# Kernel optimization log

Hardware: AMD Instinct MI355X
Metric: run time of the kernel (lower is better)

Reference implementation:

```python
import jax, jax.numpy as jnp
import numpy as np

N_HEAD = 16
EPS = 1e-6

def hypersphere_norm(x, g):
    # unit-normalize on hidden dim, rescale to sqrt(d), learnable gain
    d = x.shape[-1]
    n = jnp.linalg.norm(x, axis=-1, keepdims=True)
    return (x / (n + EPS)) * jnp.sqrt(jnp.asarray(d, x.dtype)) * g


def setup_inputs() -> dict:
    key = jax.random.key(0)
    ks = jax.random.split(key, 8)
    B, S, D, F = 2, 2048, 2048, 8192
    s = lambda fan: 1.0 / np.sqrt(fan)
    return {
        "hidden_states": jax.random.normal(ks[0], (B, S, D), jnp.float32),
        "Wq": jax.random.normal(ks[1], (D, D), jnp.float32) * s(D),
        "Wk": jax.random.normal(ks[2], (D, D), jnp.float32) * s(D),
        "Wv": jax.random.normal(ks[3], (D, D), jnp.float32) * s(D),
        "Wo": jax.random.normal(ks[4], (D, D), jnp.float32) * s(D),
        "W_in": jax.random.normal(ks[5], (F, D), jnp.float32) * s(D),
        "W_out": jax.random.normal(ks[6], (D, F), jnp.float32) * s(F),
        "qk_norm_factor": jnp.asarray(1.0 / np.sqrt(D // N_HEAD), jnp.float32),
        "g_attn": jnp.ones((D,), jnp.float32),
        "g_mlp": jnp.ones((D,), jnp.float32),
    }


def reference(hidden_states, Wq, Wk, Wv, Wo, W_in, W_out, qk_norm_factor, g_attn, g_mlp):
    B, S, D = hidden_states.shape
    H = N_HEAD
    hd = D // H

    # ---- pre-attn hypersphere norm ----
    residual = hidden_states
    x = hypersphere_norm(hidden_states, g_attn)

    def shape_heads(t):  # [B,S,D] -> [B,H,S,hd]
        return t.reshape(B, S, H, hd).transpose(0, 2, 1, 3)

    q = shape_heads(x @ Wq.T)
    k = shape_heads(x @ Wk.T)
    v = shape_heads(x @ Wv.T)

    # QK-norm: unit-normalize per head vector
    q = q / (jnp.linalg.norm(q, axis=-1, keepdims=True) + EPS)
    k = k / (jnp.linalg.norm(k, axis=-1, keepdims=True) + EPS)

    scores = jnp.einsum("bhqd,bhkd->bhqk", q, k) * qk_norm_factor
    causal = jnp.tril(jnp.ones((S, S), bool))
    scores = jnp.where(causal[None, None], scores, jnp.asarray(-jnp.inf, scores.dtype))
    probs = jax.nn.softmax(scores, axis=-1)
    attn = jnp.einsum("bhqk,bhkd->bhqd", probs, v)  # [B,H,S,hd]
    attn = attn.transpose(0, 2, 1, 3).reshape(B, S, D)
    attn = attn @ Wo.T  # dropout=0

    h = residual + attn

    # ---- MLP branch ----
    residual = h
    y = hypersphere_norm(h, g_mlp)
    y = jax.nn.gelu(y @ W_in.T, approximate=False)
    y = y @ W_out.T
    return residual + y
```

## Files before the change

### kernel.cpp

```cpp
#include <hip/hip_runtime.h>
#include <math.h>


typedef unsigned short ushort_t;
typedef __attribute__((ext_vector_type(8))) short short8;
typedef __attribute__((ext_vector_type(4))) short short4v;
typedef __attribute__((ext_vector_type(4))) float f32x4;

#define S_LEN 2048
#define D_DIM 2048
#define F_DIM 8192
#define NHEAD 16
#define HDIM 128
#define BATCH 2
#define MROWS (BATCH * S_LEN)

__device__ __forceinline__ float bf2f(ushort_t u) {
  union { unsigned int i; float f; } c; c.i = ((unsigned int)u) << 16; return c.f;
}
__device__ __forceinline__ ushort_t f2bf(float f) {
  union { unsigned int i; float f; } c; c.f = f;
  unsigned int u = c.i;
  unsigned int r = (u + 0x7FFFu + ((u >> 16) & 1u)) >> 16;
  return (ushort_t)r;
}
__device__ __forceinline__ void load_lds16(const ushort_t* g, ushort_t* l) {
  __builtin_amdgcn_global_load_lds((const __attribute__((address_space(1))) void*)g,
                                   (__attribute__((address_space(3))) void*)l,
                                   16, 0, 0);
}
__device__ __forceinline__ f32x4 mf(short8 a, short8 b, f32x4 c) {
  return __builtin_amdgcn_mfma_f32_16x16x32_bf16(a, b, c, 0, 0, 0);
}

__global__ __launch_bounds__(256) void f2b_all_kernel(const float* __restrict__ wq,
                                                      const float* __restrict__ wk,
                                                      const float* __restrict__ wv,
                                                      const float* __restrict__ wo,
                                                      const float* __restrict__ wi,
                                                      const float* __restrict__ wu,
                                                      ushort_t* __restrict__ out) {
  const size_t DD = (size_t)D_DIM * D_DIM;
  const size_t FD = (size_t)F_DIM * D_DIM;
  const size_t e = ((size_t)blockIdx.x * 256 + threadIdx.x) * 4;
  const float* src;
  size_t off;
  if (e < 4 * DD) {
    const int wsel = (int)(e >> 22);
    src = (wsel == 0) ? wq : (wsel == 1) ? wk : (wsel == 2) ? wv : wo;
    off = e & (DD - 1);
  } else if (e < 4 * DD + FD) {
    src = wi; off = e - 4 * DD;
  } else {
    src = wu; off = e - 4 * DD - FD;
  }
  float4 v = *(const float4*)(src + off);
  short4v o;
  o[0] = (short)f2bf(v.x); o[1] = (short)f2bf(v.y);
  o[2] = (short)f2bf(v.z); o[3] = (short)f2bf(v.w);
  *(short4v*)(out + e) = o;
}

__global__ __launch_bounds__(256) void hsnorm_kernel(const float* __restrict__ x,
                                                     const float* __restrict__ g,
                                                     ushort_t* __restrict__ out) {
  const int row = blockIdx.x;
  const int t = threadIdx.x;
  const size_t base = (size_t)row * D_DIM + t * 8;
  float4 x0 = *(const float4*)(x + base);
  float4 x1 = *(const float4*)(x + base + 4);
  float f[8] = {x0.x, x0.y, x0.z, x0.w, x1.x, x1.y, x1.z, x1.w};
  float ss = 0.f;
#pragma unroll
  for (int j = 0; j < 8; ++j) ss += f[j] * f[j];
#pragma unroll
  for (int o = 32; o >= 1; o >>= 1) ss += __shfl_xor(ss, o);
  __shared__ float red[4];
  if ((t & 63) == 0) red[t >> 6] = ss;
  __syncthreads();
  const float tot = red[0] + red[1] + red[2] + red[3];
  const float factor = 45.254833995939045f / (sqrtf(tot) + 1e-6f);
  float4 g0 = *(const float4*)(g + t * 8);
  float4 g1 = *(const float4*)(g + t * 8 + 4);
  float gg[8] = {g0.x, g0.y, g0.z, g0.w, g1.x, g1.y, g1.z, g1.w};
  short8 ov;
#pragma unroll
  for (int j = 0; j < 8; ++j) ov[j] = (short)f2bf(f[j] * factor * gg[j]);
  *(short8*)(out + base) = ov;
}

__global__ __launch_bounds__(256) void qknorm_kernel(ushort_t* __restrict__ buf, float scale) {
  const int wv = threadIdx.x >> 6;
  const int lane = threadIdx.x & 63;
  const size_t vi = (size_t)blockIdx.x * 4 + wv;
  ushort_t* p = buf + vi * 128 + lane * 2;
  const float a = bf2f(p[0]), b = bf2f(p[1]);
  float ss = a * a + b * b;
#pragma unroll
  for (int o = 32; o >= 1; o >>= 1) ss += __shfl_xor(ss, o);
  const float f = scale / (sqrtf(ss) + 1e-6f);
  p[0] = f2bf(a * f);
  p[1] = f2bf(b * f);
}

template <int EPI>
__global__ __launch_bounds__(512, 2) void gemm256(const ushort_t* __restrict__ A,
                                                  const ushort_t* __restrict__ W,
                                                  const float* __restrict__ RES,
                                                  void* __restrict__ Cv,
                                                  int M, int N, int K) {
  extern __shared__ char smem[];
  const int tid = threadIdx.x;
  const int w = tid >> 6;
  const int lane = tid & 63;
  const int quad = lane >> 4;
  const int l15 = lane & 15;
  const int wr = w >> 2, wc = w & 3;
  const long bm = (long)blockIdx.x * 256;
  const long bn = (long)blockIdx.y * 256;

  const int sw = l15 & 7;
  const int arow = (wr * 128 + l15) << 7;
  const int a_off0 = arow + ((quad ^ sw) << 4);
  const int a_off1 = arow + (((4 | quad) ^ sw) << 4);
  const int brow = (wc * 64 + l15) << 7;
  const int b_off0 = 65536 + brow + ((quad ^ sw) << 4);
  const int b_off1 = 65536 + brow + (((4 | quad) ^ sw) << 4);

  const int sr = tid >> 3;
  const int ss = ((tid & 7) ^ (sr & 7)) << 3;
  const ushort_t* gA = A + (size_t)(bm + sr) * K + ss;
  const ushort_t* gB = W + (size_t)(bn + sr) * K + ss;
  const size_t rstep = (size_t)64 * K;
  const int sdst = w * 1024;

#define STAGE_A(PB, GP)                                                        \
  {                                                                            \
    _Pragma("unroll") for (int ld = 0; ld < 4; ++ld)                           \
        load_lds16((GP) + ld * rstep,                                          \
                   (ushort_t*)(smem + (PB)*32768 + ld * 8192 + sdst));         \
  }
#define STAGE_B(PB, GP)                                                        \
  {                                                                            \
    _Pragma("unroll") for (int ld = 0; ld < 4; ++ld)                           \
        load_lds16((GP) + ld * rstep,                                          \
                   (ushort_t*)(smem + 65536 + (PB)*32768 + ld * 8192 + sdst)); \
  }

  f32x4 acc[8][4] = {};
  short8 af[4][2], bf[4][2];
  const int NT = K >> 6;

  STAGE_A(0, gA);
  STAGE_B(0, gB);
  STAGE_A(1, gA + 64);
  gA += 128;
  gB += 64;
  asm volatile("s_waitcnt vmcnt(4)" ::: "memory");
  __builtin_amdgcn_s_barrier();

  for (int kt0 = 0; kt0 < NT; kt0 += 2) {
#pragma unroll
    for (int pp = 0; pp < 2; ++pp) {
      const int kt = kt0 + pp;
      const char* sa = smem + pp * 32768;
#pragma unroll
      for (int i = 0; i < 4; ++i) {
        af[i][0] = *(const short8*)(sa + a_off0 + i * 2048);
        af[i][1] = *(const short8*)(sa + a_off1 + i * 2048);
      }
#pragma unroll
      for (int j = 0; j < 2; ++j) {
        bf[j][0] = *(const short8*)(sa + b_off0 + j * 2048);
        bf[j][1] = *(const short8*)(sa + b_off1 + j * 2048);
      }
      if (kt + 1 < NT) STAGE_B(1 - pp, gB);
      gB += 64;
      __builtin_amdgcn_s_barrier();
      __builtin_amdgcn_s_setprio(1);
#pragma unroll
      for (int i = 0; i < 4; ++i)
#pragma unroll
        for (int j = 0; j < 2; ++j) {
          acc[i][j] = mf(af[i][0], bf[j][0], acc[i][j]);
          acc[i][j] = mf(af[i][1], bf[j][1], acc[i][j]);
        }
      __builtin_amdgcn_s_setprio(0);
      __builtin_amdgcn_s_barrier();
#pragma unroll
      for (int j = 0; j < 2; ++j) {
        bf[2 + j][0] = *(const short8*)(sa + b_off0 + (2 + j) * 2048);
        bf[2 + j][1] = *(const short8*)(sa + b_off1 + (2 + j) * 2048);
      }
      __builtin_amdgcn_s_barrier();
      __builtin_amdgcn_s_setprio(1);
#pragma unroll
      for (int i = 0; i < 4; ++i)
#pragma unroll
        for (int j = 0; j < 2; ++j) {
          acc[i][2 + j] = mf(af[i][0], bf[2 + j][0], acc[i][2 + j]);
          acc[i][2 + j] = mf(af[i][1], bf[2 + j][1], acc[i][2 + j]);
        }
      __builtin_amdgcn_s_setprio(0);
      __builtin_amdgcn_s_barrier();
#pragma unroll
      for (int i = 0; i < 4; ++i) {
        af[i][0] = *(const short8*)(sa + a_off0 + (4 + i) * 2048);
        af[i][1] = *(const short8*)(sa + a_off1 + (4 + i) * 2048);
      }
      __builtin_amdgcn_s_barrier();
      __builtin_amdgcn_s_setprio(1);
#pragma unroll
      for (int i = 0; i < 4; ++i)
#pragma unroll
        for (int j = 0; j < 2; ++j) {
          acc[4 + i][2 + j] = mf(af[i][0], bf[2 + j][0], acc[4 + i][2 + j]);
          acc[4 + i][2 + j] = mf(af[i][1], bf[2 + j][1], acc[4 + i][2 + j]);
        }
      __builtin_amdgcn_s_setprio(0);
      __builtin_amdgcn_s_barrier();
      if (kt + 2 < NT) STAGE_A(pp, gA);
      gA += 64;
      __builtin_amdgcn_s_barrier();
      __builtin_amdgcn_s_setprio(1);
#pragma unroll
      for (int i = 0; i < 4; ++i)
#pragma unroll
        for (int j = 0; j < 2; ++j) {
          acc[4 + i][j] = mf(af[i][0], bf[j][0], acc[4 + i][j]);
          acc[4 + i][j] = mf(af[i][1], bf[j][1], acc[4 + i][j]);
        }
      __builtin_amdgcn_s_setprio(0);
      if (kt + 2 < NT) {
        asm volatile("s_waitcnt vmcnt(4)" ::: "memory");
      } else {
        asm volatile("s_waitcnt vmcnt(0)" ::: "memory");
      }
      __builtin_amdgcn_s_barrier();
    }
  }
#undef STAGE_A
#undef STAGE_B

  const size_t SZq = (size_t)MROWS * D_DIM;
#pragma unroll
  for (int i = 0; i < 8; ++i) {
    const long row0 = bm + wr * 128 + i * 16 + quad * 4;
#pragma unroll
    for (int j = 0; j < 4; ++j) {
      const long col = bn + wc * 64 + j * 16 + l15;
      if (EPI == 4) {
        if (col < 4096) {
          ushort_t* dst = (ushort_t*)Cv + (col < 2048 ? 0 : SZq);
          const long c = col & (D_DIM - 1);
#pragma unroll
          for (int r = 0; r < 4; ++r)
            dst[(size_t)(row0 + r) * D_DIM + c] = f2bf(acc[i][j][r]);
        } else {
          const long b = row0 >> 11;
          const long s0 = row0 & (S_LEN - 1);
          const long h = (col >> 7) & 15;
          const long d = col & (HDIM - 1);
          short4v ov;
#pragma unroll
          for (int r = 0; r < 4; ++r) ov[r] = (short)f2bf(acc[i][j][r]);
          *(short4v*)((ushort_t*)Cv + 2 * SZq + ((b * NHEAD + h) * HDIM + d) * S_LEN + s0) = ov;
        }
      } else {
#pragma unroll
        for (int r = 0; r < 4; ++r) {
          float v = acc[i][j][r];
          const size_t idx = (size_t)(row0 + r) * N + col;
          if (EPI == 1) {
            ((float*)Cv)[idx] = v + RES[idx];
          } else if (EPI == 2) {
            v = 0.5f * v * (1.0f + erff(v * 0.70710678118654752f));
            ((ushort_t*)Cv)[idx] = f2bf(v);
          }
        }
      }
    }
  }
}

__global__ __launch_bounds__(256) void attn_kernel(const ushort_t* __restrict__ q,
                                                   const ushort_t* __restrict__ k,
                                                   const ushort_t* __restrict__ vt,
                                                   ushort_t* __restrict__ out) {
  __shared__ __align__(16) ushort_t K_lds[64 * 128];
  __shared__ __align__(16) ushort_t Vt_lds[128 * 64];
  __shared__ __align__(16) ushort_t P_lds[4 * 16 * 64];
  const int tid = threadIdx.x;
  const int w = tid >> 6;
  const int lane = tid & 63;
  const int quad = lane >> 4;
  const int l15 = lane & 15;

  const int qt = (S_LEN / 64 - 1) - (blockIdx.x & (S_LEN / 64 - 1));
  const int bh = blockIdx.x >> 5;
  const int b = bh >> 4;
  const int h = bh & 15;
  const int q0 = qt * 64;
  const int wrow0 = q0 + w * 16;
  const size_t base = ((size_t)b * S_LEN) * D_DIM + h * HDIM;
  const size_t vtbase = ((size_t)(b * NHEAD + h)) * HDIM * S_LEN;

  short8 qa[4];
#pragma unroll
  for (int st = 0; st < 4; ++st)
    qa[st] = *(const short8*)(q + base + (size_t)(wrow0 + l15) * D_DIM + st * 32 + quad * 8);

  const int kc0 = w * 64 + lane;
  ushort_t* Pw = P_lds + w * 1024;

  f32x4 o[8] = {};
  float m[4], l[4];
#pragma unroll
  for (int r = 0; r < 4; ++r) { m[r] = -__builtin_inff(); l[r] = 0.f; }

  const int ktmax = (q0 + 63) >> 6;
  for (int kt = 0; kt <= ktmax; ++kt) {
#pragma unroll
    for (int r2 = 0; r2 < 4; ++r2) {
      const int c = r2 * 256 + kc0;
      {
        const int db = c >> 8, key = (c >> 2) & 63, dl = (c & 3) * 8;
        load_lds16(k + base + (size_t)(kt * 64 + key) * D_DIM + db * 32 + dl,
                   K_lds + (size_t)(r2 * 4 + w) * 512);
      }
      {
        const int kc = c >> 9, d = (c >> 2) & 127, kl = (c & 3) * 8;
        load_lds16(vt + vtbase + (size_t)d * S_LEN + kt * 64 + kc * 32 + kl,
                   Vt_lds + (size_t)(r2 * 4 + w) * 512);
      }
    }
    __syncthreads();

    if (kt * 64 <= wrow0 + 15) {
      f32x4 s[4];
#pragma unroll
      for (int h2 = 0; h2 < 4; ++h2) {
        f32x4 sa = {};
#pragma unroll
        for (int st = 0; st < 4; ++st) {
          short8 kb = *(const short8*)&K_lds[st * 2048 + (h2 * 16 + l15) * 32 + quad * 8];
          sa = __builtin_amdgcn_mfma_f32_16x16x32_bf16(qa[st], kb, sa, 0, 0, 0);
        }
        s[h2] = sa;
      }

      const int kbase = kt * 64 + l15;
      float alpha[4];
#pragma unroll
      for (int r = 0; r < 4; ++r) {
        const int qrow = wrow0 + quad * 4 + r;
        float sv[4];
#pragma unroll
        for (int h2 = 0; h2 < 4; ++h2)
          sv[h2] = (kbase + h2 * 16 <= qrow) ? s[h2][r] : -__builtin_inff();
        float tmax = fmaxf(fmaxf(sv[0], sv[1]), fmaxf(sv[2], sv[3]));
#pragma unroll
        for (int off = 8; off >= 1; off >>= 1) tmax = fmaxf(tmax, __shfl_xor(tmax, off));
        const float mn = fmaxf(m[r], tmax);
        const float al = __expf(m[r] - mn);
        float p[4], ps = 0.f;
#pragma unroll
        for (int h2 = 0; h2 < 4; ++h2) { p[h2] = __expf(sv[h2] - mn); ps += p[h2]; }
#pragma unroll
        for (int off = 8; off >= 1; off >>= 1) ps += __shfl_xor(ps, off);
        l[r] = l[r] * al + ps;
        m[r] = mn;
        alpha[r] = al;
#pragma unroll
        for (int h2 = 0; h2 < 4; ++h2)
          Pw[(h2 >> 1) * 512 + (quad * 4 + r) * 32 + (h2 & 1) * 16 + l15] = f2bf(p[h2]);
      }

#pragma unroll
      for (int c = 0; c < 8; ++c)
#pragma unroll
        for (int r = 0; r < 4; ++r) o[c][r] *= alpha[r];

      short8 af0 = *(const short8*)&Pw[l15 * 32 + quad * 8];
      short8 af1 = *(const short8*)&Pw[512 + l15 * 32 + quad * 8];
#pragma unroll
      for (int c = 0; c < 8; ++c) {
        short8 vb0 = *(const short8*)&Vt_lds[(c * 16 + l15) * 32 + quad * 8];
        o[c] = __builtin_amdgcn_mfma_f32_16x16x32_bf16(af0, vb0, o[c], 0, 0, 0);
        short8 vb1 = *(const short8*)&Vt_lds[4096 + (c * 16 + l15) * 32 + quad * 8];
        o[c] = __builtin_amdgcn_mfma_f32_16x16x32_bf16(af1, vb1, o[c], 0, 0, 0);
      }
    }
    __syncthreads();
  }

#pragma unroll
  for (int c = 0; c < 8; ++c)
#pragma unroll
    for (int r = 0; r < 4; ++r) {
      const float val = o[c][r] / l[r];
      out[base + (size_t)(wrow0 + quad * 4 + r) * D_DIM + c * 16 + l15] = f2bf(val);
    }
}

extern "C" void kernel_launch(void* const* d_in, const int* in_sizes, int n_in,
                              void* d_out, int out_size, void* d_ws, size_t ws_size,
                              hipStream_t stream) {
  const float* hid  = (const float*)d_in[0];
  const float* Wq   = (const float*)d_in[1];
  const float* Wk   = (const float*)d_in[2];
  const float* Wv   = (const float*)d_in[3];
  const float* Wo   = (const float*)d_in[4];
  const float* Win  = (const float*)d_in[5];
  const float* Wout = (const float*)d_in[6];
  const float* ga   = (const float*)d_in[8];
  const float* gm   = (const float*)d_in[9];
  float* out = (float*)d_out;

  const size_t DD = (size_t)D_DIM * D_DIM;
  const size_t FD = (size_t)F_DIM * D_DIM;
  const size_t SZ = (size_t)MROWS * D_DIM;

  ushort_t* wqb  = (ushort_t*)d_ws;
  ushort_t* wob  = wqb + 3 * DD;
  ushort_t* winb = wob + DD;
  ushort_t* woutb= winb + FD;
  float*    hb   = (float*)(woutb + FD);
  ushort_t* qb   = (ushort_t*)(hb + SZ);
  ushort_t* kb   = qb + SZ;
  ushort_t* vtb  = kb + SZ;
  ushort_t* xb   = vtb + SZ;
  ushort_t* mid  = kb;

  static int attr_set = 0;
  if (!attr_set) {
    hipFuncSetAttribute((const void*)&gemm256<1>,
                        hipFuncAttributeMaxDynamicSharedMemorySize, 131072);
    hipFuncSetAttribute((const void*)&gemm256<2>,
                        hipFuncAttributeMaxDynamicSharedMemorySize, 131072);
    hipFuncSetAttribute((const void*)&gemm256<4>,
                        hipFuncAttributeMaxDynamicSharedMemorySize, 131072);
    attr_set = 1;
  }

  f2b_all_kernel<<<(unsigned)((4 * DD + 2 * FD) / 1024), 256, 0, stream>>>(
      Wq, Wk, Wv, Wo, Win, Wout, wqb);

  hsnorm_kernel<<<MROWS, 256, 0, stream>>>(hid, ga, xb);
  gemm256<4><<<dim3(MROWS / 256, 6144 / 256), 512, 131072, stream>>>(
      xb, wqb, nullptr, qb, MROWS, 6144, D_DIM);
  qknorm_kernel<<<(MROWS * NHEAD) / 4, 256, 0, stream>>>(qb, 0.08838834764831845f);
  qknorm_kernel<<<(MROWS * NHEAD) / 4, 256, 0, stream>>>(kb, 1.0f);
  attn_kernel<<<BATCH * NHEAD * (S_LEN / 64), 256, 0, stream>>>(qb, kb, vtb, xb);
  gemm256<1><<<dim3(MROWS / 256, D_DIM / 256), 512, 131072, stream>>>(
      xb, wob, hid, hb, MROWS, D_DIM, D_DIM);
  hsnorm_kernel<<<MROWS, 256, 0, stream>>>(hb, gm, qb);
  gemm256<2><<<dim3(MROWS / 256, F_DIM / 256), 512, 131072, stream>>>(
      qb, winb, nullptr, mid, MROWS, F_DIM, D_DIM);
  gemm256<1><<<dim3(MROWS / 256, D_DIM / 256), 512, 131072, stream>>>(
      mid, woutb, hb, out, MROWS, D_DIM, F_DIM);
}
```

Before: 986.5 us.

## Stage GEMM tiles through registers instead of direct global-to-LDS loads

Replaces the direct global-to-LDS (buffer load to LDS) staging in the GEMM main loop with register-staged loads. A and B tiles are loaded into registers and written to the alternate LDS buffer partway through each k-step. B fragments are now reloaded from LDS instead of kept live, which cuts register pressure. The change reduces LDS buffering depth for A from two tiles ahead to one. It also adds VGPR pressure and exposes global latency within one k-step, and it relies on vmcnt waits the compiler inserts.

```diff
diff --git a/kernel.cpp b/kernel.cpp
--- a/kernel.cpp
+++ b/kernel.cpp
@@ -128,35 +128,28 @@
   const int b_off1 = 65536 + brow + (((4 | quad) ^ sw) << 4);
 
   const int sr = tid >> 3;
-  const int ss = ((tid & 7) ^ (sr & 7)) << 3;
-  const ushort_t* gA = A + (size_t)(bm + sr) * K + ss;
-  const ushort_t* gB = W + (size_t)(bn + sr) * K + ss;
+  const int cs = tid & 7;
+  const ushort_t* gA = A + (size_t)(bm + sr) * K + cs * 8;
+  const ushort_t* gB = W + (size_t)(bn + sr) * K + cs * 8;
   const size_t rstep = (size_t)64 * K;
-  const int sdst = w * 1024;
-
-#define STAGE_A(PB, GP)                                                        \
-  {                                                                            \
-    _Pragma("unroll") for (int ld = 0; ld < 4; ++ld)                           \
-        load_lds16((GP) + ld * rstep,                                          \
-                   (ushort_t*)(smem + (PB)*32768 + ld * 8192 + sdst));         \
-  }
-#define STAGE_B(PB, GP)                                                        \
-  {                                                                            \
-    _Pragma("unroll") for (int ld = 0; ld < 4; ++ld)                           \
-        load_lds16((GP) + ld * rstep,                                          \
-                   (ushort_t*)(smem + 65536 + (PB)*32768 + ld * 8192 + sdst)); \
-  }
+  const int wb = sr * 128 + ((cs ^ (sr & 7)) << 4);
 
   f32x4 acc[8][4] = {};
-  short8 af[4][2], bf[4][2];
+  short8 af[4][2], bf[2][2], aA[4], bB[4];
   const int NT = K >> 6;
 
-  STAGE_A(0, gA);
-  STAGE_B(0, gB);
-  STAGE_A(1, gA + 64);
-  gA += 128;
-  gB += 64;
-  asm volatile("s_waitcnt vmcnt(4)" ::: "memory");
+#pragma unroll
+  for (int ld = 0; ld < 4; ++ld) aA[ld] = *(const short8*)(gA + ld * rstep);
+#pragma unroll
+  for (int ld = 0; ld < 4; ++ld) bB[ld] = *(const short8*)(gB + ld * rstep);
+  gA += 64; gB += 64;
+#pragma unroll
+  for (int ld = 0; ld < 4; ++ld)
+    *(short8*)(smem + wb + ld * 8192) = aA[ld];
+#pragma unroll
+  for (int ld = 0; ld < 4; ++ld)
+    *(short8*)(smem + 65536 + wb + ld * 8192) = bB[ld];
+  asm volatile("s_waitcnt lgkmcnt(0)" ::: "memory");
   __builtin_amdgcn_s_barrier();
 
   for (int kt0 = 0; kt0 < NT; kt0 += 2) {
@@ -164,6 +157,8 @@
     for (int pp = 0; pp < 2; ++pp) {
       const int kt = kt0 + pp;
       const char* sa = smem + pp * 32768;
+      char* wbuf = smem + (1 - pp) * 32768;
+      const bool more = (kt + 1 < NT);
 #pragma unroll
       for (int i = 0; i < 4; ++i) {
         af[i][0] = *(const short8*)(sa + a_off0 + i * 2048);
@@ -174,8 +169,11 @@
         bf[j][0] = *(const short8*)(sa + b_off0 + j * 2048);
         bf[j][1] = *(const short8*)(sa + b_off1 + j * 2048);
       }
-      if (kt + 1 < NT) STAGE_B(1 - pp, gB);
-      gB += 64;
+      if (more) {
+#pragma unroll
+        for (int ld = 0; ld < 4; ++ld) aA[ld] = *(const short8*)(gA + ld * rstep);
+      }
+      gA += 64;
       __builtin_amdgcn_s_barrier();
       __builtin_amdgcn_s_setprio(1);
 #pragma unroll
@@ -189,8 +187,8 @@
       __builtin_amdgcn_s_barrier();
 #pragma unroll
       for (int j = 0; j < 2; ++j) {
-        bf[2 + j][0] = *(const short8*)(sa + b_off0 + (2 + j) * 2048);
-        bf[2 + j][1] = *(const short8*)(sa + b_off1 + (2 + j) * 2048);
+        bf[j][0] = *(const short8*)(sa + b_off0 + (2 + j) * 2048);
+        bf[j][1] = *(const short8*)(sa + b_off1 + (2 + j) * 2048);
       }
       __builtin_amdgcn_s_barrier();
       __builtin_amdgcn_s_setprio(1);
@@ -198,8 +196,8 @@
       for (int i = 0; i < 4; ++i)
 #pragma unroll
         for (int j = 0; j < 2; ++j) {
-          acc[i][2 + j] = mf(af[i][0], bf[2 + j][0], acc[i][2 + j]);
-          acc[i][2 + j] = mf(af[i][1], bf[2 + j][1], acc[i][2 + j]);
+          acc[i][2 + j] = mf(af[i][0], bf[j][0], acc[i][2 + j]);
+          acc[i][2 + j] = mf(af[i][1], bf[j][1], acc[i][2 + j]);
         }
       __builtin_amdgcn_s_setprio(0);
       __builtin_amdgcn_s_barrier();
@@ -208,19 +206,35 @@
         af[i][0] = *(const short8*)(sa + a_off0 + (4 + i) * 2048);
         af[i][1] = *(const short8*)(sa + a_off1 + (4 + i) * 2048);
       }
+      if (more) {
+#pragma unroll
+        for (int ld = 0; ld < 4; ++ld)
+          *(short8*)(wbuf + wb + ld * 8192) = aA[ld];
+#pragma unroll
+        for (int ld = 0; ld < 4; ++ld) bB[ld] = *(const short8*)(gB + ld * rstep);
+      }
+      gB += 64;
       __builtin_amdgcn_s_barrier();
       __builtin_amdgcn_s_setprio(1);
 #pragma unroll
       for (int i = 0; i < 4; ++i)
 #pragma unroll
         for (int j = 0; j < 2; ++j) {
-          acc[4 + i][2 + j] = mf(af[i][0], bf[2 + j][0], acc[4 + i][2 + j]);
-          acc[4 + i][2 + j] = mf(af[i][1], bf[2 + j][1], acc[4 + i][2 + j]);
+          acc[4 + i][2 + j] = mf(af[i][0], bf[j][0], acc[4 + i][2 + j]);
+          acc[4 + i][2 + j] = mf(af[i][1], bf[j][1], acc[4 + i][2 + j]);
         }
       __builtin_amdgcn_s_setprio(0);
       __builtin_amdgcn_s_barrier();
-      if (kt + 2 < NT) STAGE_A(pp, gA);
-      gA += 64;
+#pragma unroll
+      for (int j = 0; j < 2; ++j) {
+        bf[j][0] = *(const short8*)(sa + b_off0 + j * 2048);
+        bf[j][1] = *(const short8*)(sa + b_off1 + j * 2048);
+      }
+      if (more) {
+#pragma unroll
+        for (int ld = 0; ld < 4; ++ld)
+          *(short8*)(wbuf + 65536 + wb + ld * 8192) = bB[ld];
+      }
       __builtin_amdgcn_s_barrier();
       __builtin_amdgcn_s_setprio(1);
 #pragma unroll
@@ -231,16 +245,10 @@
           acc[4 + i][j] = mf(af[i][1], bf[j][1], acc[4 + i][j]);
         }
       __builtin_amdgcn_s_setprio(0);
-      if (kt + 2 < NT) {
-        asm volatile("s_waitcnt vmcnt(4)" ::: "memory");
-      } else {
-        asm volatile("s_waitcnt vmcnt(0)" ::: "memory");
-      }
+      asm volatile("s_waitcnt lgkmcnt(0)" ::: "memory");
       __builtin_amdgcn_s_barrier();
     }
   }
-#undef STAGE_A
-#undef STAGE_B
 
   const size_t SZq = (size_t)MROWS * D_DIM;
 #pragma unroll
```

Measured after the change: 1.098 ms. +11.3%, slower.
